# Kernel optimization log

Measured on AMD Instinct MI355X. Metric: run time of the kernel, lower is better.

Reference implementation:

```python
import jax, jax.numpy as jnp
import numpy as np

# ---- fixed structuring elements (buffers, not trainable) ----
N_SCALES = 4
BASE = 2.0
ZERO_SCALE = 1.0
PAD_VAL = 10000.0

_scales = ZERO_SCALE ** 2 * np.power(BASE, np.arange(N_SCALES)) ** 2  # t_k = 4^k
_widths = [4 * int(np.ceil(np.sqrt(s))) for s in _scales]             # 4,8,16,32
SES = [jnp.asarray([(1.0 / (4.0 * t)) * x ** 2 for x in range(-w, w + 1)],
                   dtype=jnp.float32)
       for t, w in zip(_scales, _widths)]  # SE lengths 9,17,33,65 (all odd)


def _pool1d(im, se, c, axis, is_max):
    """Weighted sliding max/min along `axis` (separable morphological op).
    out[p] = max_j padded[p+j] - c*se[j]  (dilation) or min_j padded[p+j] + c*se[j]."""
    n = se.shape[0]
    w = n // 2  # n is odd -> symmetric pad, matches torch pad1==pad2
    pad_val = -PAD_VAL if is_max else PAD_VAL
    cfg = [(0, 0)] * im.ndim
    cfg[axis] = (w, w)
    padded = jnp.pad(im, cfg, constant_values=pad_val)
    L = im.shape[axis]

    def take(j):
        return jax.lax.dynamic_slice_in_dim(padded, j, L, axis)

    win = jax.vmap(take)(jnp.arange(n))          # [n, B, C, H, W]
    se_b = se.reshape((n,) + (1,) * im.ndim)     # broadcast over image dims
    if is_max:
        return jnp.max(win - c * se_b, axis=0)
    return jnp.min(win + c * se_b, axis=0)


def _sep_dilation(im, se, c):
    tmp = _pool1d(im, se, c, axis=-1, is_max=True)   # horizontal
    return _pool1d(tmp, se, c, axis=-2, is_max=True)  # vertical


def _sep_erosion(im, se, c):
    tmp = _pool1d(im, se, c, axis=-1, is_max=False)
    return _pool1d(tmp, se, c, axis=-2, is_max=False)


def setup_inputs() -> dict:
    key = jax.random.key(0)
    k1, _ = jax.random.split(key)
    inputs = jax.random.normal(k1, (4, 8, 256, 256), dtype=jnp.float32)
    se_coef = jnp.float32(0.5)
    return {"inputs": inputs, "se_coef": se_coef}


def reference(inputs, se_coef):
    # closing = erosion(dilation(x)) per scale, stacked on new axis 2
    outs = [_sep_erosion(_sep_dilation(inputs, se, se_coef), se, se_coef)
            for se in SES]
    return jnp.stack(outs, axis=2)  # [B, C, n_scales, H, W]
```

## Files before the change

### kernel.cpp

```cpp
#include <hip/hip_runtime.h>


#define HH 256
#define WW 256
#define BC 32
#define NS 4
#define HW (HH * WW)
#define SLICE ((long)BC * HW)
#define LSTR 324

template <int W, bool IS_MAX>
__device__ __forceinline__ void hpass_lds(const float* __restrict__ lw, float cw,
                                          float acc[8])
{
    const float PAD = IS_MAX ? -1e30f : 1e30f;
#pragma unroll
    for (int pp = 0; pp < 8; ++pp) acc[pp] = PAD;
#pragma unroll
    for (int u = 0; u < (8 + 2 * W) / 2; ++u) {
        const float2 v = *(const float2*)(lw + 2 * u);
#pragma unroll
        for (int pp = 0; pp < 8; ++pp) {
            const int d1 = 2 * u - W - pp;
            const int d2 = d1 + 1;
            const bool ok1 = (d1 >= -W) && (d1 <= W);
            const bool ok2 = (d2 >= -W) && (d2 <= W);
            const float K1 = (float)(d1 * d1);
            const float K2 = (float)(d2 * d2);
            if (ok1 && ok2) {
                const float c1 = IS_MAX ? fmaf(cw, -K1, v.x) : fmaf(cw, K1, v.x);
                const float c2 = IS_MAX ? fmaf(cw, -K2, v.y) : fmaf(cw, K2, v.y);
                acc[pp] = IS_MAX ? fmaxf(fmaxf(acc[pp], c1), c2)
                                 : fminf(fminf(acc[pp], c1), c2);
            } else if (ok1) {
                const float c1 = IS_MAX ? fmaf(cw, -K1, v.x) : fmaf(cw, K1, v.x);
                acc[pp] = IS_MAX ? fmaxf(acc[pp], c1) : fminf(acc[pp], c1);
            } else if (ok2) {
                const float c2 = IS_MAX ? fmaf(cw, -K2, v.y) : fmaf(cw, K2, v.y);
                acc[pp] = IS_MAX ? fmaxf(acc[pp], c2) : fminf(acc[pp], c2);
            }
        }
    }
}

template <int W, bool IS_MAX>
__device__ __forceinline__ void vpass_core(const float* __restrict__ img, int x,
                                           int h0, float cw, float acc[8])
{
    const float PAD = IS_MAX ? -1e30f : 1e30f;
#pragma unroll
    for (int pp = 0; pp < 8; ++pp) acc[pp] = PAD;
#pragma unroll
    for (int ch = 0; ch < (8 + 2 * W) / 8; ++ch) {
        float v[8];
#pragma unroll
        for (int q = 0; q < 8; ++q) {
            const int h = h0 + ch * 8 + q - W;
            const int hc = min(max(h, 0), HH - 1);
            const float tv = img[(long)hc * WW + x];
            v[q] = (h == hc) ? tv : PAD;
        }
#pragma unroll
        for (int pp = 0; pp < 8; ++pp) {
#pragma unroll
            for (int q = 0; q < 8; q += 2) {
                const int d1 = ch * 8 + q - W - pp;
                const int d2 = d1 + 1;
                const bool ok1 = (d1 >= -W) && (d1 <= W);
                const bool ok2 = (d2 >= -W) && (d2 <= W);
                const float K1 = (float)(d1 * d1);
                const float K2 = (float)(d2 * d2);
                if (ok1 && ok2) {
                    const float c1 = IS_MAX ? fmaf(cw, -K1, v[q])     : fmaf(cw, K1, v[q]);
                    const float c2 = IS_MAX ? fmaf(cw, -K2, v[q + 1]) : fmaf(cw, K2, v[q + 1]);
                    acc[pp] = IS_MAX ? fmaxf(fmaxf(acc[pp], c1), c2)
                                     : fminf(fminf(acc[pp], c1), c2);
                } else if (ok1) {
                    const float c1 = IS_MAX ? fmaf(cw, -K1, v[q]) : fmaf(cw, K1, v[q]);
                    acc[pp] = IS_MAX ? fmaxf(acc[pp], c1) : fminf(acc[pp], c1);
                } else if (ok2) {
                    const float c2 = IS_MAX ? fmaf(cw, -K2, v[q + 1]) : fmaf(cw, K2, v[q + 1]);
                    acc[pp] = IS_MAX ? fmaxf(acc[pp], c2) : fminf(acc[pp], c2);
                }
            }
        }
    }
}

template <int W>
__device__ __forceinline__ void dh_impl(const float* __restrict__ ip,
                                        float* __restrict__ op_base,
                                        float c, float* lbuf)
{
    const int tid = threadIdx.x;
    const int r = tid >> 5, t = tid & 31;
    const int row = blockIdx.y * 8 + r;
    const float cw = c * (4.0f / (float)(W * W));

    const float* rowp = ip + (long)row * WW;
    float4 v0 = *(const float4*)(rowp + 4 * t);
    float4 v1 = *(const float4*)(rowp + 128 + 4 * t);
    float* lr = lbuf + r * LSTR;
    *(float4*)(lr + W + 4 * t) = v0;
    *(float4*)(lr + W + 128 + 4 * t) = v1;
    if (t < W) { lr[t] = -1e30f; lr[W + 256 + t] = -1e30f; }
    __syncthreads();

    float acc[8];
    hpass_lds<W, true>(lr + 8 * t, cw, acc);
    float* op = op_base + (long)row * WW + 8 * t;
    *(float4*)(op)     = make_float4(acc[0], acc[1], acc[2], acc[3]);
    *(float4*)(op + 4) = make_float4(acc[4], acc[5], acc[6], acc[7]);
}

__global__ __launch_bounds__(256, 4) void k1_dh(const float* __restrict__ in,
                                                float* __restrict__ out,
                                                const float* __restrict__ cptr,
                                                long in_ks, long in_zs,
                                                long out_ks, long out_zs)
{
    __shared__ float lbuf[8 * LSTR];
    const int k = blockIdx.z, z = blockIdx.x;
    const float c = cptr[0];
    const float* ip = in + (long)k * in_ks + (long)z * in_zs;
    float* op = out + (long)k * out_ks + (long)z * out_zs;
    switch (k) {
        case 0: dh_impl<4 >(ip, op, c, lbuf); break;
        case 1: dh_impl<8 >(ip, op, c, lbuf); break;
        case 2: dh_impl<16>(ip, op, c, lbuf); break;
        case 3: dh_impl<32>(ip, op, c, lbuf); break;
    }
}

template <int W>
__device__ __forceinline__ void dveh_impl(const float* __restrict__ img,
                                          float* __restrict__ op_base,
                                          float c, float* lbuf)
{
    const int x = threadIdx.x;
    const int h0 = blockIdx.y * 8;
    const float cw = c * (4.0f / (float)(W * W));

    float vacc[8];
    vpass_core<W, true>(img, x, h0, cw, vacc);

#pragma unroll
    for (int q = 0; q < 8; ++q) lbuf[q * LSTR + W + x] = vacc[q];
    if (x < W) {
#pragma unroll
        for (int q = 0; q < 8; ++q) {
            lbuf[q * LSTR + x] = 1e30f;
            lbuf[q * LSTR + W + 256 + x] = 1e30f;
        }
    }
    __syncthreads();

    const int r = threadIdx.x >> 5, t = threadIdx.x & 31;
    float acc[8];
    hpass_lds<W, false>(lbuf + r * LSTR + 8 * t, cw, acc);
    float* op = op_base + (long)(h0 + r) * WW + 8 * t;
    *(float4*)(op)     = make_float4(acc[0], acc[1], acc[2], acc[3]);
    *(float4*)(op + 4) = make_float4(acc[4], acc[5], acc[6], acc[7]);
}

__global__ __launch_bounds__(256, 4) void k2_dveh(const float* __restrict__ in,
                                                  float* __restrict__ out,
                                                  const float* __restrict__ cptr,
                                                  long in_ks, long in_zs,
                                                  long out_ks, long out_zs)
{
    __shared__ float lbuf[8 * LSTR];
    const int k = blockIdx.z, z = blockIdx.x;
    const float c = cptr[0];
    const float* ip = in + (long)k * in_ks + (long)z * in_zs;
    float* op = out + (long)k * out_ks + (long)z * out_zs;
    switch (k) {
        case 0: dveh_impl<4 >(ip, op, c, lbuf); break;
        case 1: dveh_impl<8 >(ip, op, c, lbuf); break;
        case 2: dveh_impl<16>(ip, op, c, lbuf); break;
        case 3: dveh_impl<32>(ip, op, c, lbuf); break;
    }
}

template <int W>
__device__ __forceinline__ void ev_impl(const float* __restrict__ img,
                                        float* __restrict__ op_base, float c)
{
    const int x = threadIdx.x;
    const int h0 = blockIdx.y * 8;
    const float cw = c * (4.0f / (float)(W * W));
    float acc[8];
    vpass_core<W, false>(img, x, h0, cw, acc);
#pragma unroll
    for (int pp = 0; pp < 8; ++pp)
        op_base[(long)(h0 + pp) * WW + x] = acc[pp];
}

__global__ __launch_bounds__(256, 4) void k3_ev(const float* __restrict__ in,
                                                float* __restrict__ out,
                                                const float* __restrict__ cptr,
                                                long in_ks, long in_zs,
                                                long out_ks, long out_zs)
{
    const int k = blockIdx.z, z = blockIdx.x;
    const float c = cptr[0];
    const float* ip = in + (long)k * in_ks + (long)z * in_zs;
    float* op = out + (long)k * out_ks + (long)z * out_zs;
    switch (k) {
        case 0: ev_impl<4 >(ip, op, c); break;
        case 1: ev_impl<8 >(ip, op, c); break;
        case 2: ev_impl<16>(ip, op, c); break;
        case 3: ev_impl<32>(ip, op, c); break;
    }
}

extern "C" void kernel_launch(void* const* d_in, const int* in_sizes, int n_in,
                              void* d_out, int out_size, void* d_ws, size_t ws_size,
                              hipStream_t stream)
{
    const float* x = (const float*)d_in[0];
    const float* c = (const float*)d_in[1];
    float* out = (float*)d_out;
    float* ws  = (float*)d_ws;

    dim3 b(256);
    if (ws_size >= (size_t)(NS * SLICE) * sizeof(float)) {
        dim3 g(BC, HH / 8, NS);
        k1_dh  <<<g, b, 0, stream>>>(x,   out, c, 0,     HW, HW,    (long)NS * HW);
        k2_dveh<<<g, b, 0, stream>>>(out, ws,  c, HW,    (long)NS * HW, SLICE, HW);
        k3_ev  <<<g, b, 0, stream>>>(ws,  out, c, SLICE, HW, HW,    (long)NS * HW);
    } else {
        dim3 g(BC, HH / 8, 1);
        for (int k = 0; k < NS; ++k) {
            float* outk = out + (long)k * HW;
            dim3 gz(BC, HH / 8, 1);
            switch (k) {
                case 0:
                    k1_dh  <<<gz, b, 0, stream>>>(x,    outk, c, 0, HW, 0, (long)NS * HW);
                    k2_dveh<<<gz, b, 0, stream>>>(outk, ws,   c, 0, (long)NS * HW, 0, HW);
                    k3_ev  <<<gz, b, 0, stream>>>(ws,   outk, c, 0, HW, 0, (long)NS * HW);
                    break;
                default: {
                    dim3 gk(BC, HH / 8, (unsigned)(k + 1));
                    k1_dh  <<<gk, b, 0, stream>>>(x,   out, c, 0, HW, HW, (long)NS * HW);
                    k2_dveh<<<gk, b, 0, stream>>>(out, ws,  c, HW, (long)NS * HW,
                                                  (long)(ws_size / sizeof(float) / (k + 1) / (BC * HW)) ? SLICE : 0, HW);
                    k3_ev  <<<gk, b, 0, stream>>>(ws,  out, c, (long)(ws_size / sizeof(float) / (k + 1) / (BC * HW)) ? SLICE : 0, HW, HW, (long)NS * HW);
                    break;
                }
            }
        }
    }
}
```

Baseline: 123.7 us.

## Fuse separable passes into two vertical+horizontal kernels with k-innermost block order

Replaces the three-kernel pipeline (horizontal dilation, fused vertical-dilation+horizontal-erosion, vertical erosion) with two launches of one templated kernel. Each launch does a vertical pass followed by a horizontal pass through LDS, covering first the whole dilation and then the whole erosion. This drops one full intermediate write and read to global memory. It also flattens the grid to 1D so the four scales of the same image tile run in adjacent blocks, which should improve L2 reuse of the shared input. In exchange the load is less balanced, because blocks with the widest element sit next to blocks with the narrowest, and the fallback paths for small workspace now launch many more kernels.

```diff
diff --git a/kernel.cpp b/kernel.cpp
--- a/kernel.cpp
+++ b/kernel.cpp
@@ -87,130 +87,61 @@
     }
 }
 
-template <int W>
-__device__ __forceinline__ void dh_impl(const float* __restrict__ ip,
+template <int W, bool IS_MAX>
+__device__ __forceinline__ void vh_impl(const float* __restrict__ img,
                                         float* __restrict__ op_base,
-                                        float c, float* lbuf)
-{
-    const int tid = threadIdx.x;
-    const int r = tid >> 5, t = tid & 31;
-    const int row = blockIdx.y * 8 + r;
-    const float cw = c * (4.0f / (float)(W * W));
-
-    const float* rowp = ip + (long)row * WW;
-    float4 v0 = *(const float4*)(rowp + 4 * t);
-    float4 v1 = *(const float4*)(rowp + 128 + 4 * t);
-    float* lr = lbuf + r * LSTR;
-    *(float4*)(lr + W + 4 * t) = v0;
-    *(float4*)(lr + W + 128 + 4 * t) = v1;
-    if (t < W) { lr[t] = -1e30f; lr[W + 256 + t] = -1e30f; }
-    __syncthreads();
-
-    float acc[8];
-    hpass_lds<W, true>(lr + 8 * t, cw, acc);
-    float* op = op_base + (long)row * WW + 8 * t;
-    *(float4*)(op)     = make_float4(acc[0], acc[1], acc[2], acc[3]);
-    *(float4*)(op + 4) = make_float4(acc[4], acc[5], acc[6], acc[7]);
-}
-
-__global__ __launch_bounds__(256, 4) void k1_dh(const float* __restrict__ in,
-                                                float* __restrict__ out,
-                                                const float* __restrict__ cptr,
-                                                long in_ks, long in_zs,
-                                                long out_ks, long out_zs)
-{
-    __shared__ float lbuf[8 * LSTR];
-    const int k = blockIdx.z, z = blockIdx.x;
-    const float c = cptr[0];
-    const float* ip = in + (long)k * in_ks + (long)z * in_zs;
-    float* op = out + (long)k * out_ks + (long)z * out_zs;
-    switch (k) {
-        case 0: dh_impl<4 >(ip, op, c, lbuf); break;
-        case 1: dh_impl<8 >(ip, op, c, lbuf); break;
-        case 2: dh_impl<16>(ip, op, c, lbuf); break;
-        case 3: dh_impl<32>(ip, op, c, lbuf); break;
-    }
-}
-
-template <int W>
-__device__ __forceinline__ void dveh_impl(const float* __restrict__ img,
-                                          float* __restrict__ op_base,
-                                          float c, float* lbuf)
+                                        int h0, float c, float* lbuf)
 {
     const int x = threadIdx.x;
-    const int h0 = blockIdx.y * 8;
     const float cw = c * (4.0f / (float)(W * W));
+    const float PAD = IS_MAX ? -1e30f : 1e30f;
 
     float vacc[8];
-    vpass_core<W, true>(img, x, h0, cw, vacc);
+    vpass_core<W, IS_MAX>(img, x, h0, cw, vacc);
 
 #pragma unroll
     for (int q = 0; q < 8; ++q) lbuf[q * LSTR + W + x] = vacc[q];
     if (x < W) {
 #pragma unroll
         for (int q = 0; q < 8; ++q) {
-            lbuf[q * LSTR + x] = 1e30f;
-            lbuf[q * LSTR + W + 256 + x] = 1e30f;
+            lbuf[q * LSTR + x] = PAD;
+            lbuf[q * LSTR + W + 256 + x] = PAD;
         }
     }
     __syncthreads();
 
     const int r = threadIdx.x >> 5, t = threadIdx.x & 31;
     float acc[8];
-    hpass_lds<W, false>(lbuf + r * LSTR + 8 * t, cw, acc);
+    hpass_lds<W, IS_MAX>(lbuf + r * LSTR + 8 * t, cw, acc);
     float* op = op_base + (long)(h0 + r) * WW + 8 * t;
     *(float4*)(op)     = make_float4(acc[0], acc[1], acc[2], acc[3]);
     *(float4*)(op + 4) = make_float4(acc[4], acc[5], acc[6], acc[7]);
 }
 
-__global__ __launch_bounds__(256, 4) void k2_dveh(const float* __restrict__ in,
-                                                  float* __restrict__ out,
-                                                  const float* __restrict__ cptr,
-                                                  long in_ks, long in_zs,
-                                                  long out_ks, long out_zs)
+template <bool IS_MAX>
+__global__ __launch_bounds__(256, 4) void k_vh(const float* __restrict__ in,
+                                               float* __restrict__ out,
+                                               const float* __restrict__ cptr,
+                                               long in_ks, long in_zs,
+                                               long out_ks, long out_zs,
+                                               int kbase, int kbits,
+                                               int zbase, int zbits)
 {
     __shared__ float lbuf[8 * LSTR];
-    const int k = blockIdx.z, z = blockIdx.x;
+    const int bid = blockIdx.x;
+    const int k = kbase + (bid & ((1 << kbits) - 1));
+    const int rest = bid >> kbits;
+    const int z = zbase + (rest & ((1 << zbits) - 1));
+    const int y = rest >> zbits;
+    const int h0 = y * 8;
     const float c = cptr[0];
     const float* ip = in + (long)k * in_ks + (long)z * in_zs;
     float* op = out + (long)k * out_ks + (long)z * out_zs;
     switch (k) {
-        case 0: dveh_impl<4 >(ip, op, c, lbuf); break;
-        case 1: dveh_impl<8 >(ip, op, c, lbuf); break;
-        case 2: dveh_impl<16>(ip, op, c, lbuf); break;
-        case 3: dveh_impl<32>(ip, op, c, lbuf); break;
-    }
-}
-
-template <int W>
-__device__ __forceinline__ void ev_impl(const float* __restrict__ img,
-                                        float* __restrict__ op_base, float c)
-{
-    const int x = threadIdx.x;
-    const int h0 = blockIdx.y * 8;
-    const float cw = c * (4.0f / (float)(W * W));
-    float acc[8];
-    vpass_core<W, false>(img, x, h0, cw, acc);
-#pragma unroll
-    for (int pp = 0; pp < 8; ++pp)
-        op_base[(long)(h0 + pp) * WW + x] = acc[pp];
-}
-
-__global__ __launch_bounds__(256, 4) void k3_ev(const float* __restrict__ in,
-                                                float* __restrict__ out,
-                                                const float* __restrict__ cptr,
-                                                long in_ks, long in_zs,
-                                                long out_ks, long out_zs)
-{
-    const int k = blockIdx.z, z = blockIdx.x;
-    const float c = cptr[0];
-    const float* ip = in + (long)k * in_ks + (long)z * in_zs;
-    float* op = out + (long)k * out_ks + (long)z * out_zs;
-    switch (k) {
-        case 0: ev_impl<4 >(ip, op, c); break;
-        case 1: ev_impl<8 >(ip, op, c); break;
-        case 2: ev_impl<16>(ip, op, c); break;
-        case 3: ev_impl<32>(ip, op, c); break;
+        case 0: vh_impl<4,  IS_MAX>(ip, op, h0, c, lbuf); break;
+        case 1: vh_impl<8,  IS_MAX>(ip, op, h0, c, lbuf); break;
+        case 2: vh_impl<16, IS_MAX>(ip, op, h0, c, lbuf); break;
+        case 3: vh_impl<32, IS_MAX>(ip, op, h0, c, lbuf); break;
     }
 }
 
@@ -224,31 +155,29 @@
     float* ws  = (float*)d_ws;
 
     dim3 b(256);
-    if (ws_size >= (size_t)(NS * SLICE) * sizeof(float)) {
-        dim3 g(BC, HH / 8, NS);
-        k1_dh  <<<g, b, 0, stream>>>(x,   out, c, 0,     HW, HW,    (long)NS * HW);
-        k2_dveh<<<g, b, 0, stream>>>(out, ws,  c, HW,    (long)NS * HW, SLICE, HW);
-        k3_ev  <<<g, b, 0, stream>>>(ws,  out, c, SLICE, HW, HW,    (long)NS * HW);
+    const size_t slice_b = (size_t)SLICE * sizeof(float);
+    if (ws_size >= (size_t)NS * slice_b) {
+        dim3 g(NS * BC * (HH / 8));
+        k_vh<true ><<<g, b, 0, stream>>>(x,  ws,  c, 0,     HW, SLICE, HW,
+                                         0, 2, 0, 5);
+        k_vh<false><<<g, b, 0, stream>>>(ws, out, c, SLICE, HW, HW, (long)NS * HW,
+                                         0, 2, 0, 5);
+    } else if (ws_size >= slice_b) {
+        dim3 g(BC * (HH / 8));
+        for (int k = 0; k < NS; ++k) {
+            k_vh<true ><<<g, b, 0, stream>>>(x,  ws,  c, 0, HW, 0, HW,
+                                             k, 0, 0, 5);
+            k_vh<false><<<g, b, 0, stream>>>(ws, out, c, 0, HW, HW, (long)NS * HW,
+                                             k, 0, 0, 5);
+        }
     } else {
-        dim3 g(BC, HH / 8, 1);
-        for (int k = 0; k < NS; ++k) {
-            float* outk = out + (long)k * HW;
-            dim3 gz(BC, HH / 8, 1);
-            switch (k) {
-                case 0:
-                    k1_dh  <<<gz, b, 0, stream>>>(x,    outk, c, 0, HW, 0, (long)NS * HW);
-                    k2_dveh<<<gz, b, 0, stream>>>(outk, ws,   c, 0, (long)NS * HW, 0, HW);
-                    k3_ev  <<<gz, b, 0, stream>>>(ws,   outk, c, 0, HW, 0, (long)NS * HW);
-                    break;
-                default: {
-                    dim3 gk(BC, HH / 8, (unsigned)(k + 1));
-                    k1_dh  <<<gk, b, 0, stream>>>(x,   out, c, 0, HW, HW, (long)NS * HW);
-                    k2_dveh<<<gk, b, 0, stream>>>(out, ws,  c, HW, (long)NS * HW,
-                                                  (long)(ws_size / sizeof(float) / (k + 1) / (BC * HW)) ? SLICE : 0, HW);
-                    k3_ev  <<<gk, b, 0, stream>>>(ws,  out, c, (long)(ws_size / sizeof(float) / (k + 1) / (BC * HW)) ? SLICE : 0, HW, HW, (long)NS * HW);
-                    break;
-                }
+        dim3 g(HH / 8);
+        for (int k = 0; k < NS; ++k)
+            for (int z = 0; z < BC; ++z) {
+                k_vh<true ><<<g, b, 0, stream>>>(x,  ws,  c, 0, HW, 0, 0,
+                                                 k, 0, z, 0);
+                k_vh<false><<<g, b, 0, stream>>>(ws, out, c, 0, 0, HW, (long)NS * HW,
+                                                 k, 0, z, 0);
             }
-        }
     }
 }
```

Result: slower. 143.1 us (+15.7%).
